# Performance work log

Hardware: AMD Instinct MI355X
Metric: run time of the kernel (lower is better)

Reference implementation:

```python
import jax, jax.numpy as jnp
import numpy as np

B, LQ, DM, DFFN, NL, NH, NP = 4, 13294, 256, 1024, 4, 8, 4
HD = DM // NH
SHAPES = np.array([[100, 100], [50, 50], [25, 25], [13, 13]], dtype=np.int64)


def _ln(x, g, b):
    m = x.mean(-1, keepdims=True)
    v = ((x - m) ** 2).mean(-1, keepdims=True)
    return (x - m) / jnp.sqrt(v + 1e-5) * g + b


def _ms_deform(value, loc, aw, shapes):
    # value: [B, Lv, NH, HD]; loc: [B, Lq, NH, NL, NP, 2]; aw: [B, Lq, NH, NL, NP]
    Bn, Lq = loc.shape[0], loc.shape[1]
    offs = np.concatenate([[0], np.cumsum(shapes[:, 0] * shapes[:, 1])])
    out = jnp.zeros((Bn, NH, Lq, HD), value.dtype)
    for l in range(NL):
        H, W = int(shapes[l, 0]), int(shapes[l, 1])
        val = value[:, offs[l]:offs[l + 1]].transpose(0, 2, 1, 3)  # [B,NH,HW,HD]
        # grid_sample align_corners=False convention: pixel = norm*size - 0.5
        x = (loc[:, :, :, l, :, 0] * W - 0.5).transpose(0, 2, 1, 3).reshape(Bn, NH, Lq * NP)
        y = (loc[:, :, :, l, :, 1] * H - 0.5).transpose(0, 2, 1, 3).reshape(Bn, NH, Lq * NP)
        x0 = jnp.floor(x); y0 = jnp.floor(y)
        fx = x - x0; fy = y - y0
        acc = jnp.zeros((Bn, NH, Lq * NP, HD), value.dtype)
        for dy, dx in ((0, 0), (0, 1), (1, 0), (1, 1)):
            xi = x0 + dx; yi = y0 + dy
            w = (fx if dx else 1.0 - fx) * (fy if dy else 1.0 - fy)
            valid = (xi >= 0) & (xi < W) & (yi >= 0) & (yi < H)  # zero padding
            idx = (jnp.clip(yi, 0, H - 1) * W + jnp.clip(xi, 0, W - 1)).astype(jnp.int32)
            g = jnp.take_along_axis(val, idx[..., None], axis=2)  # [B,NH,Lq*NP,HD]
            acc = acc + g * (w * valid)[..., None]
        a = aw[:, :, :, l].transpose(0, 2, 1, 3).reshape(Bn, NH, Lq * NP)
        out = out + (acc * a[..., None]).reshape(Bn, NH, Lq, NP, HD).sum(3)
    return out.transpose(0, 2, 1, 3).reshape(Bn, Lq, NH * HD)


def _forward(src, pos, reference_points, shapes, Wv, bv, Ws, bs, Wa, ba, Wo, bo,
             W1, b1, W2, b2, g1, be1, g2, be2):
    Bn, Lq, _ = src.shape
    q = src + pos
    value = (src @ Wv + bv).reshape(Bn, Lq, NH, HD)
    off = (q @ Ws + bs).reshape(Bn, Lq, NH, NL, NP, 2)
    aw = jax.nn.softmax((q @ Wa + ba).reshape(Bn, Lq, NH, NL * NP), axis=-1)
    aw = aw.reshape(Bn, Lq, NH, NL, NP)
    norm = jnp.asarray(np.ascontiguousarray(shapes[:, ::-1]), jnp.float32)  # (W,H) per level
    loc = reference_points[:, :, None, :, None, :] + off / norm[None, None, None, :, None, :]
    attn = _ms_deform(value, loc, aw, shapes) @ Wo + bo
    x = _ln(src + attn, g1, be1)
    h = jax.nn.relu(x @ W1 + b1)
    return _ln(x + h @ W2 + b2, g2, be2)


def setup_inputs():
    key = jax.random.key(0)
    ks = jax.random.split(key, 12)

    def lin(k, i, o):
        k1, k2 = jax.random.split(k)
        return (0.02 * jax.random.normal(k1, (i, o), jnp.float32),
                0.02 * jax.random.normal(k2, (o,), jnp.float32))

    Wv, bv = lin(ks[0], DM, DM)
    Ws, bs = lin(ks[1], DM, NH * NL * NP * 2)
    Wa, ba = lin(ks[2], DM, NH * NL * NP)
    Wo, bo = lin(ks[3], DM, DM)
    W1, b1 = lin(ks[4], DM, DFFN)
    W2, b2 = lin(ks[5], DFFN, DM)
    lsi = np.concatenate([[0], np.cumsum(SHAPES[:, 0] * SHAPES[:, 1])[:-1]])
    return {
        "src": jax.random.normal(ks[6], (B, LQ, DM), jnp.float32),
        "pos": jax.random.normal(ks[7], (B, LQ, DM), jnp.float32),
        "reference_points": jax.random.uniform(ks[8], (B, LQ, NL, 2), jnp.float32),
        "spatial_shapes": jnp.asarray(SHAPES),
        "level_start_index": jnp.asarray(lsi),
        "Wv": Wv, "bv": bv, "Ws": Ws, "bs": bs, "Wa": Wa, "ba": ba,
        "Wo": Wo, "bo": bo, "W1": W1, "b1": b1, "W2": W2, "b2": b2,
        "g1": jnp.ones((DM,), jnp.float32), "be1": jnp.zeros((DM,), jnp.float32),
        "g2": jnp.ones((DM,), jnp.float32), "be2": jnp.zeros((DM,), jnp.float32),
    }


def reference(src, pos, reference_points, spatial_shapes, level_start_index,
              Wv, bv, Ws, bs, Wa, ba, Wo, bo, W1, b1, W2, b2, g1, be1, g2, be2):
    shapes = np.asarray(spatial_shapes)
    return _forward(src, pos, reference_points, shapes, Wv, bv, Ws, bs, Wa, ba,
                    Wo, bo, W1, b1, W2, b2, g1, be1, g2, be2)
```

## Files before the change

kernel.cpp:

```cpp
#include <hip/hip_runtime.h>


#define LQn   13294
#define MREAL 53176
#define MP    53248
#define MHALF 26588

typedef __attribute__((ext_vector_type(8))) short short8;
typedef __attribute__((ext_vector_type(4))) short short4v;
typedef __attribute__((ext_vector_type(4))) float f32x4;
typedef __attribute__((ext_vector_type(2))) float f32x2;

__device__ __forceinline__ short f2bf(float f) {
    unsigned u = __float_as_uint(f);
    unsigned r = (u + 0x7FFFu + ((u >> 16) & 1u)) >> 16;
    return (short)r;
}
__device__ __forceinline__ float bf2f(short b) {
    return __uint_as_float(((unsigned)(unsigned short)b) << 16);
}
__device__ __forceinline__ f32x2 bf2x2(unsigned r) {
    f32x2 o;
    o.x = __uint_as_float(r << 16);
    o.y = __uint_as_float(r & 0xffff0000u);
    return o;
}

#define GLOAD16(gp, lp)                                                        \
    __builtin_amdgcn_global_load_lds(                                          \
        (const __attribute__((address_space(1))) void*)(gp),                   \
        (__attribute__((address_space(3))) void*)(lp), 16, 0, 0)

__global__ __launch_bounds__(256) void prep_all(
    const float* __restrict__ Wv, const float* __restrict__ Ws,
    const float* __restrict__ Wa, const float* __restrict__ Wo,
    const float* __restrict__ W1, const float* __restrict__ W2,
    const float* __restrict__ bs, const float* __restrict__ ba,
    const float* __restrict__ src, const float* __restrict__ pos,
    short* __restrict__ WvT, short* __restrict__ WsaT,
    short* __restrict__ WoT, short* __restrict__ W1T,
    short* __restrict__ W2T, float* __restrict__ bsa,
    short* __restrict__ q_bf, short* __restrict__ src_bf) {
    const int bid = blockIdx.x, tid = threadIdx.x;
    if (bid >= 2945) {
        const int i = (bid - 2945) * 256 + tid;
        if (i < MREAL * 32) {
            const float4 a0 = ((const float4*)src)[i * 2];
            const float4 a1 = ((const float4*)src)[i * 2 + 1];
            const float4 b0 = ((const float4*)pos)[i * 2];
            const float4 b1 = ((const float4*)pos)[i * 2 + 1];
            short8 o, o2;
            o[0] = f2bf(a0.x + b0.x); o[1] = f2bf(a0.y + b0.y);
            o[2] = f2bf(a0.z + b0.z); o[3] = f2bf(a0.w + b0.w);
            o[4] = f2bf(a1.x + b1.x); o[5] = f2bf(a1.y + b1.y);
            o[6] = f2bf(a1.z + b1.z); o[7] = f2bf(a1.w + b1.w);
            o2[0] = f2bf(a0.x); o2[1] = f2bf(a0.y);
            o2[2] = f2bf(a0.z); o2[3] = f2bf(a0.w);
            o2[4] = f2bf(a1.x); o2[5] = f2bf(a1.y);
            o2[6] = f2bf(a1.z); o2[7] = f2bf(a1.w);
            ((short8*)q_bf)[i] = o;
            ((short8*)src_bf)[i] = o2;
        }
        return;
    }
    const float* W; short* WT; int K, N, base;
    if (bid < 256)       { W = Wv; WT = WvT;              K = 256;  N = 256;  base = 0; }
    else if (bid < 512)  { W = Ws; WT = WsaT;             K = 256;  N = 256;  base = 256; }
    else if (bid < 640)  { W = Wa; WT = WsaT + 256 * 256; K = 256;  N = 128;  base = 512; }
    else if (bid < 896)  { W = Wo; WT = WoT;              K = 256;  N = 256;  base = 640; }
    else if (bid < 1920) { W = W1; WT = W1T;              K = 256;  N = 1024; base = 896; }
    else if (bid < 2944) { W = W2; WT = W2T;              K = 1024; N = 256;  base = 1920; }
    else {
        if (tid < 256) bsa[tid] = bs[tid];
        else if (tid < 384) bsa[tid] = ba[tid - 256];
        return;
    }
    const int i = (bid - base) * 256 + tid;
    const int n = i / K, k = i - n * K;
    WT[i] = f2bf(W[(size_t)k * N + n]);
}

template <int EPI, int NT>
__device__ __forceinline__ void gemm_body(short* lA, short* lB,
                                          const short* __restrict__ Ab,
                                          const short* __restrict__ BT,
                                          const float* __restrict__ bias,
                                          void* C, int d,
                                          int M, int K, int N,
                                          int ldb, int ldc) {
    const int c = d & 7, j = d >> 3;
    const int jg = j / NT;
    const int m0 = (c + 8 * jg) * 128;
    const int n0 = (j - jg * NT) * 128;
    const int t = threadIdx.x;
    const int wid = t >> 6, lane = t & 63;
    const int wr = wid >> 1, wc = wid & 1;
    const int quad = lane >> 4, l16 = lane & 15;

    f32x4 acc[4][4];
#pragma unroll
    for (int i = 0; i < 4; ++i)
#pragma unroll
        for (int jj = 0; jj < 4; ++jj) acc[i][jj] = (f32x4){0.f, 0.f, 0.f, 0.f};

    const int grow = wid * 32 + (lane >> 2);
    const int gcol = (lane & 3) * 8;
    auto stage = [&](int buf, int k0) {
        GLOAD16(Ab + (size_t)(m0 + grow) * K + k0 + gcol,
                &lA[buf * 4096 + (wid * 32) * 32]);
        GLOAD16(Ab + (size_t)(m0 + grow + 16) * K + k0 + gcol,
                &lA[buf * 4096 + (wid * 32 + 16) * 32]);
        GLOAD16(BT + (size_t)(n0 + grow) * ldb + k0 + gcol,
                &lB[buf * 4096 + (wid * 32) * 32]);
        GLOAD16(BT + (size_t)(n0 + grow + 16) * ldb + k0 + gcol,
                &lB[buf * 4096 + (wid * 32 + 16) * 32]);
    };
    stage(0, 0);
    __syncthreads();
    int cur = 0;
    for (int k0 = 0; k0 < K; k0 += 32) {
        if (k0 + 32 < K) stage(cur ^ 1, k0 + 32);
        short8 af[4], bfr[4];
#pragma unroll
        for (int mi = 0; mi < 4; ++mi)
            af[mi] = *(const short8*)&lA[cur * 4096 + (wr * 64 + mi * 16 + l16) * 32 + quad * 8];
#pragma unroll
        for (int ni = 0; ni < 4; ++ni)
            bfr[ni] = *(const short8*)&lB[cur * 4096 + (wc * 64 + ni * 16 + l16) * 32 + quad * 8];
#pragma unroll
        for (int mi = 0; mi < 4; ++mi)
#pragma unroll
            for (int ni = 0; ni < 4; ++ni)
                acc[mi][ni] = __builtin_amdgcn_mfma_f32_16x16x32_bf16(
                    af[mi], bfr[ni], acc[mi][ni], 0, 0, 0);
        __syncthreads();
        cur ^= 1;
    }

    short* lflat = lA;
#pragma unroll
    for (int p = 0; p < 2; ++p) {
        if (wc == p) {
#pragma unroll
            for (int ni = 0; ni < 4; ++ni) {
                const int lc = ni * 16 + l16;
                const float bia = bias[n0 + p * 64 + lc];
#pragma unroll
                for (int mi = 0; mi < 4; ++mi)
#pragma unroll
                    for (int r = 0; r < 4; ++r) {
                        const int lr = wr * 64 + mi * 16 + quad * 4 + r;
                        float v = acc[mi][ni][r] + bia;
                        if (EPI == 2) v = fmaxf(v, 0.f);
                        lflat[lr * 64 + (lc ^ ((lr & 7) << 3))] = f2bf(v);
                    }
            }
        }
        __syncthreads();
#pragma unroll
        for (int i = 0; i < 4; ++i) {
            const int chunk = i * 256 + t;
            const int row = chunk >> 3;
            const int c8 = (chunk & 7) * 8;
            const int gr = m0 + row;
            if (gr < M) {
                const short8 v8 =
                    *(const short8*)&lflat[row * 64 + (c8 ^ ((row & 7) << 3))];
                const int gcl = n0 + p * 64 + c8;
                if (EPI == 5) {
                    const int b = gr / LQn, s = gr - b * LQn;
                    const int hh = gcl >> 5, dd = gcl & 31;
                    *(short8*)&((short*)C)[(((size_t)b * 8 + hh) * LQn + s) * 32 + dd] = v8;
                } else {
                    *(short8*)&((short*)C)[(size_t)gr * ldc + gcl] = v8;
                }
            }
        }
        __syncthreads();
    }
}

template <int EPI, int NT>
__global__ __launch_bounds__(256) void gemm_bt(const short* __restrict__ Ab,
                                               const short* __restrict__ BT,
                                               const float* __restrict__ bias,
                                               void* C, int M, int K, int N,
                                               int ldb, int ldc) {
    __shared__ short sA[2 * 128 * 32];
    __shared__ short sB[2 * 128 * 32];
    gemm_body<EPI, NT>(sA, sB, Ab, BT, bias, C, blockIdx.x, M, K, N, ldb, ldc);
}

__global__ __launch_bounds__(256) void gemm12(const short* __restrict__ src_bf,
                                              const short* __restrict__ WvT,
                                              const float* __restrict__ bv,
                                              short* __restrict__ value_h,
                                              const short* __restrict__ q_bf,
                                              const short* __restrict__ WsaT,
                                              const float* __restrict__ bsa,
                                              short* __restrict__ offaw) {
    __shared__ short sA[2 * 128 * 32];
    __shared__ short sB[2 * 128 * 32];
    if (blockIdx.x < 832)
        gemm_body<5, 2>(sA, sB, src_bf, WvT, bv, value_h, blockIdx.x,
                        MREAL, 256, 256, 256, 256);
    else
        gemm_body<1, 3>(sA, sB, q_bf, WsaT, bsa, offaw, blockIdx.x - 832,
                        MREAL, 256, 384, 256, 384);
}

template <int EPI>
__global__ __launch_bounds__(512) void gemm_ln(const short* __restrict__ Ab,
                                               const short* __restrict__ BT,
                                               const float* __restrict__ bias,
                                               const void* __restrict__ resid,
                                               void* __restrict__ out,
                                               const float* __restrict__ g,
                                               const float* __restrict__ be,
                                               int M, int K, int resbf) {
    const int t = threadIdx.x;
    const int m0 = blockIdx.x * 64;
    const int wid = t >> 6, lane = t & 63;
    const int wr = wid >> 2, wc = wid & 3;
    const int quad = lane >> 4, l16 = lane & 15;

    __shared__ short lA[2][64 * 32];
    __shared__ short lB[2][256 * 32];
    __shared__ float2 part[64][4];
    __shared__ float2 stats[64];

    f32x4 acc[2][4];
#pragma unroll
    for (int i = 0; i < 2; ++i)
#pragma unroll
        for (int j = 0; j < 4; ++j) acc[i][j] = (f32x4){0.f, 0.f, 0.f, 0.f};

    const int gb_row = wid * 32 + (lane >> 2);
    const int gcol8 = (lane & 3) * 8;
    auto stage = [&](int buf, int k0) {
        if (wid < 4)
            GLOAD16(Ab + (size_t)(m0 + wid * 16 + (lane >> 2)) * K + k0 + gcol8,
                    &lA[buf][(wid * 16) * 32]);
        GLOAD16(BT + (size_t)gb_row * K + k0 + gcol8,
                &lB[buf][(wid * 32) * 32]);
        GLOAD16(BT + (size_t)(gb_row + 16) * K + k0 + gcol8,
                &lB[buf][(wid * 32 + 16) * 32]);
    };
    stage(0, 0);
    __syncthreads();
    int cur = 0;
    for (int k0 = 0; k0 < K; k0 += 32) {
        if (k0 + 32 < K) stage(cur ^ 1, k0 + 32);
        short8 af[2], bfr[4];
#pragma unroll
        for (int mi = 0; mi < 2; ++mi)
            af[mi] = *(const short8*)&lA[cur][(wr * 32 + mi * 16 + l16) * 32 + quad * 8];
#pragma unroll
        for (int ni = 0; ni < 4; ++ni)
            bfr[ni] = *(const short8*)&lB[cur][(wc * 64 + ni * 16 + l16) * 32 + quad * 8];
#pragma unroll
        for (int mi = 0; mi < 2; ++mi)
#pragma unroll
            for (int ni = 0; ni < 4; ++ni)
                acc[mi][ni] = __builtin_amdgcn_mfma_f32_16x16x32_bf16(
                    af[mi], bfr[ni], acc[mi][ni], 0, 0, 0);
        __syncthreads();
        cur ^= 1;
    }

    float biasv[4], gv[4], bev[4];
    int gcs[4];
#pragma unroll
    for (int ni = 0; ni < 4; ++ni) {
        gcs[ni] = wc * 64 + ni * 16 + l16;
        biasv[ni] = bias[gcs[ni]];
        gv[ni] = g[gcs[ni]];
        bev[ni] = be[gcs[ni]];
    }
#pragma unroll
    for (int mi = 0; mi < 2; ++mi) {
#pragma unroll
        for (int r = 0; r < 4; ++r) {
            const int lr = wr * 32 + mi * 16 + quad * 4 + r;
            const int gr = m0 + lr;
            const bool ok = (gr < M);
            float s1 = 0.f, s2 = 0.f;
#pragma unroll
            for (int ni = 0; ni < 4; ++ni) {
                float v = acc[mi][ni][r] + biasv[ni];
                if (ok) {
                    if (resbf)
                        v += bf2f(((const short*)resid)[(size_t)gr * 256 + gcs[ni]]);
                    else
                        v += ((const float*)resid)[(size_t)gr * 256 + gcs[ni]];
                }
                acc[mi][ni][r] = v;
                s1 += v;
                s2 += v * v;
            }
#pragma unroll
            for (int o = 1; o < 16; o <<= 1) {
                s1 += __shfl_xor(s1, o);
                s2 += __shfl_xor(s2, o);
            }
            if (l16 == 0) part[lr][wc] = make_float2(s1, s2);
        }
    }
    __syncthreads();
    if (t < 64) {
        float s1 = 0.f, s2 = 0.f;
#pragma unroll
        for (int w = 0; w < 4; ++w) {
            const float2 p = part[t][w];
            s1 += p.x;
            s2 += p.y;
        }
        const float mean = s1 * (1.0f / 256.0f);
        const float var = s2 * (1.0f / 256.0f) - mean * mean;
        stats[t] = make_float2(mean, rsqrtf(var + 1e-5f));
    }
    __syncthreads();

    if (EPI == 0) {
        short* lflat = (short*)lA;
#pragma unroll
        for (int p = 0; p < 4; ++p) {
            if (wc == p) {
#pragma unroll
                for (int mi = 0; mi < 2; ++mi)
#pragma unroll
                    for (int r = 0; r < 4; ++r) {
                        const int lr = wr * 32 + mi * 16 + quad * 4 + r;
                        const float2 st = stats[lr];
#pragma unroll
                        for (int ni = 0; ni < 4; ++ni) {
                            const int lc = ni * 16 + l16;
                            const float v =
                                (acc[mi][ni][r] - st.x) * st.y * gv[ni] + bev[ni];
                            lflat[lr * 64 + (lc ^ ((lr & 7) << 3))] = f2bf(v);
                        }
                    }
            }
            __syncthreads();
            {
                const int row = t >> 3;
                const int c8 = (t & 7) * 8;
                const int gr = m0 + row;
                if (gr < M) {
                    const short8 v8 =
                        *(const short8*)&lflat[row * 64 + (c8 ^ ((row & 7) << 3))];
                    *(short8*)&((short*)out)[(size_t)gr * 256 + p * 64 + c8] = v8;
                }
            }
            __syncthreads();
        }
    } else {
#pragma unroll
        for (int mi = 0; mi < 2; ++mi) {
#pragma unroll
            for (int r = 0; r < 4; ++r) {
                const int lr = wr * 32 + mi * 16 + quad * 4 + r;
                const int gr = m0 + lr;
                if (gr < M) {
                    const float2 st = stats[lr];
#pragma unroll
                    for (int ni = 0; ni < 4; ++ni) {
                        const float v =
                            (acc[mi][ni][r] - st.x) * st.y * gv[ni] + bev[ni];
                        ((float*)out)[(size_t)gr * 256 + gcs[ni]] = v;
                    }
                }
            }
        }
    }
}

__global__ __launch_bounds__(256) void sample_k(const short* __restrict__ value,
                                                const short* __restrict__ offaw,
                                                const float* __restrict__ refp,
                                                short* __restrict__ attn,
                                                int nwg) {
    int wg = blockIdx.x;
    {
        const int q = nwg >> 3, r = nwg & 7;
        const int xcd = wg & 7, idx = wg >> 3;
        wg = (xcd < r ? xcd * (q + 1) : r * (q + 1) + (xcd - r) * q) + idx;
    }
    const int tid = threadIdx.x;
    const int grp = wg * 16 + (tid >> 4);
    const int s16 = tid & 15;
    const int l = s16 >> 2, sub = s16 & 3;
    const int row = grp >> 3, h = grp & 7;
    const int b = row / LQn;
    const int L = (l == 0) ? 100 : (l == 1) ? 50 : (l == 2) ? 25 : 13;
    const int O = (l == 0) ? 0 : (l == 1) ? 10000 : (l == 2) ? 12500 : 13125;
    const float Lf = (float)L;

    const short* op = offaw + (size_t)row * 384 + h * 32;
    const short* ap = offaw + (size_t)row * 384 + 256 + h * 16;

    const short4v alog = *(const short4v*)(ap + l * 4);
    float lg[4];
#pragma unroll
    for (int j = 0; j < 4; ++j) lg[j] = bf2f(alog[j]);
    float m = fmaxf(fmaxf(lg[0], lg[1]), fmaxf(lg[2], lg[3]));
    m = fmaxf(m, __shfl_xor(m, 4));
    m = fmaxf(m, __shfl_xor(m, 8));
    float s = 0.f;
#pragma unroll
    for (int j = 0; j < 4; ++j) { lg[j] = __expf(lg[j] - m); s += lg[j]; }
    s += __shfl_xor(s, 4);
    s += __shfl_xor(s, 8);
    const float inv = 1.f / s;

    const float2 rxy = *(const float2*)(refp + (size_t)row * 8 + l * 2);
    const short8 ov = *(const short8*)(op + l * 8);
    const short* vlev = value + ((size_t)(b * 8 + h) * LQn + O) * 32 + sub * 8;

    f32x2 acc2[4];
#pragma unroll
    for (int j = 0; j < 4; ++j) acc2[j] = (f32x2){0.f, 0.f};

#pragma unroll 2
    for (int p = 0; p < 4; ++p) {
        const float x = fmaf(rxy.x, Lf, bf2f(ov[p * 2 + 0]) - 0.5f);
        const float y = fmaf(rxy.y, Lf, bf2f(ov[p * 2 + 1]) - 0.5f);
        const float xf = floorf(x), yf = floorf(y);
        const int ix = (int)xf, iy = (int)yf;
        const float fx = x - xf, fy = y - yf;
        const float aw = lg[p] * inv;
        const float vx0 = ((unsigned)ix < (unsigned)L) ? 1.f : 0.f;
        const float vx1 = ((unsigned)(ix + 1) < (unsigned)L) ? 1.f : 0.f;
        const float vy0 = ((unsigned)iy < (unsigned)L) ? 1.f : 0.f;
        const float vy1 = ((unsigned)(iy + 1) < (unsigned)L) ? 1.f : 0.f;
        const float gx0 = (1.f - fx) * aw, gx1 = fx * aw;
        const float w00 = gx0 * (1.f - fy) * vx0 * vy0;
        const float w10 = gx1 * (1.f - fy) * vx1 * vy0;
        const float w01 = gx0 * fy * vx0 * vy1;
        const float w11 = gx1 * fy * vx1 * vy1;
        const int ix0 = min(max(ix, 0), L - 1);
        const int ix1 = min(max(ix + 1, 0), L - 1);
        const int iy0 = min(max(iy, 0), L - 1);
        const int iy1 = min(max(iy + 1, 0), L - 1);
        const int ro0 = iy0 * L, ro1 = iy1 * L;
        const uint4 c00 = *(const uint4*)(vlev + ((ro0 + ix0) << 5));
        const uint4 c10 = *(const uint4*)(vlev + ((ro0 + ix1) << 5));
        const uint4 c01 = *(const uint4*)(vlev + ((ro1 + ix0) << 5));
        const uint4 c11 = *(const uint4*)(vlev + ((ro1 + ix1) << 5));
        const unsigned* p00 = (const unsigned*)&c00;
        const unsigned* p10 = (const unsigned*)&c10;
        const unsigned* p01 = (const unsigned*)&c01;
        const unsigned* p11 = (const unsigned*)&c11;
#pragma unroll
        for (int j = 0; j < 4; ++j)
            acc2[j] += w00 * bf2x2(p00[j]) + w10 * bf2x2(p10[j]) +
                       w01 * bf2x2(p01[j]) + w11 * bf2x2(p11[j]);
    }

    float acc[8];
#pragma unroll
    for (int j = 0; j < 4; ++j) {
        acc[j * 2] = acc2[j].x;
        acc[j * 2 + 1] = acc2[j].y;
    }
#pragma unroll
    for (int j = 0; j < 8; ++j) {
        acc[j] += __shfl_xor(acc[j], 4);
        acc[j] += __shfl_xor(acc[j], 8);
    }

    if (l == 0) {
        short8 o;
#pragma unroll
        for (int j = 0; j < 8; ++j) o[j] = f2bf(acc[j]);
        *(short8*)(attn + (size_t)row * 256 + h * 32 + sub * 8) = o;
    }
}

extern "C" void kernel_launch(void* const* d_in, const int* in_sizes, int n_in,
                              void* d_out, int out_size, void* d_ws, size_t ws_size,
                              hipStream_t stream) {
    (void)in_sizes; (void)n_in; (void)out_size;
    const float* src  = (const float*)d_in[0];
    const float* pos  = (const float*)d_in[1];
    const float* refp = (const float*)d_in[2];
    const float* Wv = (const float*)d_in[5];
    const float* bv = (const float*)d_in[6];
    const float* Ws = (const float*)d_in[7];
    const float* bs = (const float*)d_in[8];
    const float* Wa = (const float*)d_in[9];
    const float* ba = (const float*)d_in[10];
    const float* Wo = (const float*)d_in[11];
    const float* bo = (const float*)d_in[12];
    const float* W1 = (const float*)d_in[13];
    const float* b1 = (const float*)d_in[14];
    const float* W2 = (const float*)d_in[15];
    const float* b2 = (const float*)d_in[16];
    const float* g1 = (const float*)d_in[17];
    const float* be1 = (const float*)d_in[18];
    const float* g2 = (const float*)d_in[19];
    const float* be2 = (const float*)d_in[20];

    char* ws = (char*)d_ws;
    size_t off = 0;
    auto take = [&](size_t bytes) {
        char* p = ws + off;
        off += (bytes + 255) & ~(size_t)255;
        return p;
    };
    short* WvT  = (short*)take(256 * 256 * 2);
    short* WsaT = (short*)take(384 * 256 * 2);
    short* WoT  = (short*)take(256 * 256 * 2);
    short* W1T  = (short*)take(1024 * 256 * 2);
    short* W2T  = (short*)take(256 * 1024 * 2);
    float* bsa  = (float*)take(384 * 4);

    const size_t SZ_VH = (size_t)MP * 256 * 2;
    const size_t SZ_OF = (size_t)MP * 384 * 2;
    const size_t SZ_H  = (size_t)MP * 1024 * 2;
    const size_t SZ_HX = SZ_H - (SZ_OF + 2 * SZ_VH);

    short* value_h = (short*)take(SZ_VH);
    short* offaw   = (short*)take(SZ_OF);
    short* attn_bf = (short*)take(SZ_VH);

    const size_t rem = (off <= ws_size) ? ws_size - off : 0;
    const bool cfgFull = rem >= SZ_VH + SZ_HX + 512;
    const bool cfgA    = !cfgFull && rem >= SZ_VH + 256;
    short* src_bf;
    int resbf_g4;
    if (cfgFull) {
        src_bf = (short*)take(SZ_VH);
        (void)take(SZ_HX);
        resbf_g4 = 1;
    } else if (cfgA) {
        src_bf = (short*)take(SZ_VH);
        resbf_g4 = 1;
    } else {
        src_bf = offaw;
        resbf_g4 = 0;
    }

    short* q_bf = attn_bf;
    short* x_bf = value_h;
    short* h    = offaw;
    float* z    = (float*)d_out;

    prep_all<<<9593, 256, 0, stream>>>(Wv, Ws, Wa, Wo, W1, W2, bs, ba, src, pos,
                                       WvT, WsaT, WoT, W1T, W2T, bsa, q_bf,
                                       src_bf);
    gemm12<<<2080, 256, 0, stream>>>(src_bf, WvT, bv, value_h,
                                     q_bf, WsaT, bsa, offaw);
    {
        const int nwg = (MREAL * 8) / 16;
        sample_k<<<nwg, 256, 0, stream>>>(value_h, offaw, refp, attn_bf, nwg);
    }
    gemm_ln<0><<<MP / 64, 512, 0, stream>>>(attn_bf, WoT, bo,
                                            resbf_g4 ? (const void*)src_bf
                                                     : (const void*)src,
                                            x_bf, g1, be1, MREAL, 256, resbf_g4);
    if (cfgFull) {
        gemm_bt<2, 8><<<3328, 256, 0, stream>>>(
            x_bf, W1T, b1, h, MREAL, 256, 1024, 256, 1024);
        gemm_ln<1><<<MP / 64, 512, 0, stream>>>(h, W2T, b2, x_bf, z, g2, be2,
                                                MREAL, 1024, 1);
    } else {
        for (int half = 0; half < 2; ++half) {
            const size_t ro = (size_t)half * MHALF;
            gemm_bt<2, 8><<<1664, 256, 0, stream>>>(
                x_bf + ro * 256, W1T, b1, h, MHALF, 256, 1024, 256, 1024);
            gemm_ln<1><<<(MHALF + 63) / 64, 512, 0, stream>>>(
                h, W2T, b2, x_bf + ro * 256, z + ro * 256, g2, be2, MHALF, 1024,
                1);
        }
    }
}
```

Baseline: 366.4 us.

## Fuse FFN up-projection, ReLU, down-projection and LayerNorm into one kernel

Replaces the separate W1 GEMM (writing a 1024-wide bf16 hidden buffer to global memory) and the W2 GEMM+LayerNorm kernel with a single kernel. Each 64-row block computes hidden chunks of 128 columns into shared memory and immediately accumulates them into the W2 output, avoiding the large hidden-tensor round trip and the workspace-size branches. In exchange, x rows are read directly from global per MFMA step, weights are restreamed for every row block, and the per-block tile is small (64 rows), which may lower MFMA efficiency relative to the standalone tiled GEMM.

```diff
diff --git a/kernel.cpp b/kernel.cpp
--- a/kernel.cpp
+++ b/kernel.cpp
@@ -4,7 +4,6 @@
 #define LQn   13294
 #define MREAL 53176
 #define MP    53248
-#define MHALF 26588
 
 typedef __attribute__((ext_vector_type(8))) short short8;
 typedef __attribute__((ext_vector_type(4))) short short4v;
@@ -151,7 +150,6 @@
                     for (int r = 0; r < 4; ++r) {
                         const int lr = wr * 64 + mi * 16 + quad * 4 + r;
                         float v = acc[mi][ni][r] + bia;
-                        if (EPI == 2) v = fmaxf(v, 0.f);
                         lflat[lr * 64 + (lc ^ ((lr & 7) << 3))] = f2bf(v);
                     }
             }
@@ -180,17 +178,6 @@
     }
 }
 
-template <int EPI, int NT>
-__global__ __launch_bounds__(256) void gemm_bt(const short* __restrict__ Ab,
-                                               const short* __restrict__ BT,
-                                               const float* __restrict__ bias,
-                                               void* C, int M, int K, int N,
-                                               int ldb, int ldc) {
-    __shared__ short sA[2 * 128 * 32];
-    __shared__ short sB[2 * 128 * 32];
-    gemm_body<EPI, NT>(sA, sB, Ab, BT, bias, C, blockIdx.x, M, K, N, ldb, ldc);
-}
-
 __global__ __launch_bounds__(256) void gemm12(const short* __restrict__ src_bf,
                                               const short* __restrict__ WvT,
                                               const float* __restrict__ bv,
@@ -209,15 +196,14 @@
                         MREAL, 256, 384, 256, 384);
 }
 
-template <int EPI>
-__global__ __launch_bounds__(512) void gemm_ln(const short* __restrict__ Ab,
-                                               const short* __restrict__ BT,
-                                               const float* __restrict__ bias,
-                                               const void* __restrict__ resid,
-                                               void* __restrict__ out,
-                                               const float* __restrict__ g,
-                                               const float* __restrict__ be,
-                                               int M, int K, int resbf) {
+__global__ __launch_bounds__(512) void gemm_ln0(const short* __restrict__ Ab,
+                                                const short* __restrict__ BT,
+                                                const float* __restrict__ bias,
+                                                const void* __restrict__ resid,
+                                                void* __restrict__ out,
+                                                const float* __restrict__ g,
+                                                const float* __restrict__ be,
+                                                int M, int K, int resbf) {
     const int t = threadIdx.x;
     const int m0 = blockIdx.x * 64;
     const int wid = t >> 6, lane = t & 63;
@@ -321,54 +307,216 @@
     }
     __syncthreads();
 
-    if (EPI == 0) {
-        short* lflat = (short*)lA;
-#pragma unroll
-        for (int p = 0; p < 4; ++p) {
-            if (wc == p) {
-#pragma unroll
-                for (int mi = 0; mi < 2; ++mi)
-#pragma unroll
-                    for (int r = 0; r < 4; ++r) {
-                        const int lr = wr * 32 + mi * 16 + quad * 4 + r;
-                        const float2 st = stats[lr];
-#pragma unroll
-                        for (int ni = 0; ni < 4; ++ni) {
-                            const int lc = ni * 16 + l16;
-                            const float v =
-                                (acc[mi][ni][r] - st.x) * st.y * gv[ni] + bev[ni];
-                            lflat[lr * 64 + (lc ^ ((lr & 7) << 3))] = f2bf(v);
-                        }
-                    }
-            }
-            __syncthreads();
-            {
-                const int row = t >> 3;
-                const int c8 = (t & 7) * 8;
-                const int gr = m0 + row;
-                if (gr < M) {
-                    const short8 v8 =
-                        *(const short8*)&lflat[row * 64 + (c8 ^ ((row & 7) << 3))];
-                    *(short8*)&((short*)out)[(size_t)gr * 256 + p * 64 + c8] = v8;
-                }
-            }
-            __syncthreads();
-        }
-    } else {
-#pragma unroll
-        for (int mi = 0; mi < 2; ++mi) {
-#pragma unroll
-            for (int r = 0; r < 4; ++r) {
-                const int lr = wr * 32 + mi * 16 + quad * 4 + r;
-                const int gr = m0 + lr;
-                if (gr < M) {
+    short* lflat = (short*)lA;
+#pragma unroll
+    for (int p = 0; p < 4; ++p) {
+        if (wc == p) {
+#pragma unroll
+            for (int mi = 0; mi < 2; ++mi)
+#pragma unroll
+                for (int r = 0; r < 4; ++r) {
+                    const int lr = wr * 32 + mi * 16 + quad * 4 + r;
                     const float2 st = stats[lr];
 #pragma unroll
                     for (int ni = 0; ni < 4; ++ni) {
+                        const int lc = ni * 16 + l16;
                         const float v =
                             (acc[mi][ni][r] - st.x) * st.y * gv[ni] + bev[ni];
-                        ((float*)out)[(size_t)gr * 256 + gcs[ni]] = v;
+                        lflat[lr * 64 + (lc ^ ((lr & 7) << 3))] = f2bf(v);
                     }
+                }
+        }
+        __syncthreads();
+        {
+            const int row = t >> 3;
+            const int c8 = (t & 7) * 8;
+            const int gr = m0 + row;
+            if (gr < M) {
+                const short8 v8 =
+                    *(const short8*)&lflat[row * 64 + (c8 ^ ((row & 7) << 3))];
+                *(short8*)&((short*)out)[(size_t)gr * 256 + p * 64 + c8] = v8;
+            }
+        }
+        __syncthreads();
+    }
+}
+
+__global__ __launch_bounds__(512) void ffn_fused(const short* __restrict__ x,
+                                                 const short* __restrict__ W1T,
+                                                 const float* __restrict__ b1,
+                                                 const short* __restrict__ W2T,
+                                                 const float* __restrict__ b2,
+                                                 float* __restrict__ z,
+                                                 const float* __restrict__ g,
+                                                 const float* __restrict__ be,
+                                                 int M) {
+    const int t = threadIdx.x;
+    const int m0 = blockIdx.x * 64;
+    const int wid = t >> 6, lane = t & 63;
+    const int wr = wid >> 2, wc = wid & 3;
+    const int quad = lane >> 4, l16 = lane & 15;
+    const int s_row = lane >> 2, s_col8 = (lane & 3) * 8;
+
+    __shared__ short lW1[2][128 * 32];
+    __shared__ short lW2[2][256 * 32];
+    __shared__ short lH[64 * 128];
+    __shared__ float2 part[64][4];
+    __shared__ float2 stats[64];
+
+    f32x4 acc2[2][4];
+#pragma unroll
+    for (int i = 0; i < 2; ++i)
+#pragma unroll
+        for (int j = 0; j < 4; ++j) acc2[i][j] = (f32x4){0.f, 0.f, 0.f, 0.f};
+
+    int xrow[2];
+#pragma unroll
+    for (int mi = 0; mi < 2; ++mi)
+        xrow[mi] = min(m0 + wr * 32 + mi * 16 + l16, M - 1);
+
+    for (int nc = 0; nc < 8; ++nc) {
+        f32x4 acc1[2][2];
+#pragma unroll
+        for (int i = 0; i < 2; ++i)
+#pragma unroll
+            for (int j = 0; j < 2; ++j) acc1[i][j] = (f32x4){0.f, 0.f, 0.f, 0.f};
+
+        auto stage1 = [&](int buf, int kk) {
+            GLOAD16(W1T + (size_t)(nc * 128 + wid * 16 + s_row) * 256 + kk * 32 + s_col8,
+                    &lW1[buf][(wid * 16) * 32]);
+        };
+        stage1(0, 0);
+        __syncthreads();
+        int cur = 0;
+#pragma unroll
+        for (int kk = 0; kk < 8; ++kk) {
+            if (kk < 7) stage1(cur ^ 1, kk + 1);
+            short8 ax[2];
+#pragma unroll
+            for (int mi = 0; mi < 2; ++mi)
+                ax[mi] = *(const short8*)&x[(size_t)xrow[mi] * 256 + kk * 32 + quad * 8];
+            short8 bw[2];
+#pragma unroll
+            for (int ni = 0; ni < 2; ++ni)
+                bw[ni] = *(const short8*)&lW1[cur][((wc & 3) * 32 + ni * 16 + l16) * 32 + quad * 8];
+#pragma unroll
+            for (int mi = 0; mi < 2; ++mi)
+#pragma unroll
+                for (int ni = 0; ni < 2; ++ni)
+                    acc1[mi][ni] = __builtin_amdgcn_mfma_f32_16x16x32_bf16(
+                        ax[mi], bw[ni], acc1[mi][ni], 0, 0, 0);
+            __syncthreads();
+            cur ^= 1;
+        }
+#pragma unroll
+        for (int mi = 0; mi < 2; ++mi)
+#pragma unroll
+            for (int ni = 0; ni < 2; ++ni) {
+                const int col = wc * 32 + ni * 16 + l16;
+                const float bia = b1[nc * 128 + col];
+#pragma unroll
+                for (int r = 0; r < 4; ++r) {
+                    const int row = wr * 32 + mi * 16 + quad * 4 + r;
+                    const float v = fmaxf(acc1[mi][ni][r] + bia, 0.f);
+                    lH[row * 128 + ((((col >> 3) ^ (row & 7)) << 3) | (col & 7))] =
+                        f2bf(v);
+                }
+            }
+        __syncthreads();
+        auto stage2 = [&](int buf, int kk) {
+            GLOAD16(W2T + (size_t)(wid * 32 + s_row) * 1024 + nc * 128 + kk * 32 + s_col8,
+                    &lW2[buf][(wid * 32) * 32]);
+            GLOAD16(W2T + (size_t)(wid * 32 + 16 + s_row) * 1024 + nc * 128 + kk * 32 + s_col8,
+                    &lW2[buf][(wid * 32 + 16) * 32]);
+        };
+        stage2(0, 0);
+        __syncthreads();
+        cur = 0;
+#pragma unroll
+        for (int kk = 0; kk < 4; ++kk) {
+            if (kk < 3) stage2(cur ^ 1, kk + 1);
+            short8 ah[2];
+#pragma unroll
+            for (int mi = 0; mi < 2; ++mi) {
+                const int row = wr * 32 + mi * 16 + l16;
+                ah[mi] = *(const short8*)&lH[row * 128 +
+                                             (((kk * 4 + quad) ^ (row & 7)) << 3)];
+            }
+            short8 bw2[4];
+#pragma unroll
+            for (int ni = 0; ni < 4; ++ni)
+                bw2[ni] = *(const short8*)&lW2[cur][(wc * 64 + ni * 16 + l16) * 32 + quad * 8];
+#pragma unroll
+            for (int mi = 0; mi < 2; ++mi)
+#pragma unroll
+                for (int ni = 0; ni < 4; ++ni)
+                    acc2[mi][ni] = __builtin_amdgcn_mfma_f32_16x16x32_bf16(
+                        ah[mi], bw2[ni], acc2[mi][ni], 0, 0, 0);
+            __syncthreads();
+            cur ^= 1;
+        }
+    }
+
+    float biasv[4], gv[4], bev[4];
+    int gcs[4];
+#pragma unroll
+    for (int ni = 0; ni < 4; ++ni) {
+        gcs[ni] = wc * 64 + ni * 16 + l16;
+        biasv[ni] = b2[gcs[ni]];
+        gv[ni] = g[gcs[ni]];
+        bev[ni] = be[gcs[ni]];
+    }
+#pragma unroll
+    for (int mi = 0; mi < 2; ++mi) {
+#pragma unroll
+        for (int r = 0; r < 4; ++r) {
+            const int lr = wr * 32 + mi * 16 + quad * 4 + r;
+            const int gr = m0 + lr;
+            const bool ok = (gr < M);
+            float s1 = 0.f, s2 = 0.f;
+#pragma unroll
+            for (int ni = 0; ni < 4; ++ni) {
+                float v = acc2[mi][ni][r] + biasv[ni];
+                if (ok) v += bf2f(x[(size_t)gr * 256 + gcs[ni]]);
+                acc2[mi][ni][r] = v;
+                s1 += v;
+                s2 += v * v;
+            }
+#pragma unroll
+            for (int o = 1; o < 16; o <<= 1) {
+                s1 += __shfl_xor(s1, o);
+                s2 += __shfl_xor(s2, o);
+            }
+            if (l16 == 0) part[lr][wc] = make_float2(s1, s2);
+        }
+    }
+    __syncthreads();
+    if (t < 64) {
+        float s1 = 0.f, s2 = 0.f;
+#pragma unroll
+        for (int w = 0; w < 4; ++w) {
+            const float2 p = part[t][w];
+            s1 += p.x;
+            s2 += p.y;
+        }
+        const float mean = s1 * (1.0f / 256.0f);
+        const float var = s2 * (1.0f / 256.0f) - mean * mean;
+        stats[t] = make_float2(mean, rsqrtf(var + 1e-5f));
+    }
+    __syncthreads();
+#pragma unroll
+    for (int mi = 0; mi < 2; ++mi) {
+#pragma unroll
+        for (int r = 0; r < 4; ++r) {
+            const int lr = wr * 32 + mi * 16 + quad * 4 + r;
+            const int gr = m0 + lr;
+            if (gr < M) {
+                const float2 st = stats[lr];
+#pragma unroll
+                for (int ni = 0; ni < 4; ++ni) {
+                    const float v =
+                        (acc2[mi][ni][r] - st.x) * st.y * gv[ni] + bev[ni];
+                    z[(size_t)gr * 256 + gcs[ni]] = v;
                 }
             }
         }
@@ -517,23 +665,15 @@
 
     const size_t SZ_VH = (size_t)MP * 256 * 2;
     const size_t SZ_OF = (size_t)MP * 384 * 2;
-    const size_t SZ_H  = (size_t)MP * 1024 * 2;
-    const size_t SZ_HX = SZ_H - (SZ_OF + 2 * SZ_VH);
 
     short* value_h = (short*)take(SZ_VH);
     short* offaw   = (short*)take(SZ_OF);
     short* attn_bf = (short*)take(SZ_VH);
 
     const size_t rem = (off <= ws_size) ? ws_size - off : 0;
-    const bool cfgFull = rem >= SZ_VH + SZ_HX + 512;
-    const bool cfgA    = !cfgFull && rem >= SZ_VH + 256;
     short* src_bf;
     int resbf_g4;
-    if (cfgFull) {
-        src_bf = (short*)take(SZ_VH);
-        (void)take(SZ_HX);
-        resbf_g4 = 1;
-    } else if (cfgA) {
+    if (rem >= SZ_VH + 256) {
         src_bf = (short*)take(SZ_VH);
         resbf_g4 = 1;
     } else {
@@ -543,7 +683,6 @@
 
     short* q_bf = attn_bf;
     short* x_bf = value_h;
-    short* h    = offaw;
     float* z    = (float*)d_out;
 
     prep_all<<<9593, 256, 0, stream>>>(Wv, Ws, Wa, Wo, W1, W2, bs, ba, src, pos,
@@ -555,23 +694,10 @@
         const int nwg = (MREAL * 8) / 16;
         sample_k<<<nwg, 256, 0, stream>>>(value_h, offaw, refp, attn_bf, nwg);
     }
-    gemm_ln<0><<<MP / 64, 512, 0, stream>>>(attn_bf, WoT, bo,
-                                            resbf_g4 ? (const void*)src_bf
-                                                     : (const void*)src,
-                                            x_bf, g1, be1, MREAL, 256, resbf_g4);
-    if (cfgFull) {
-        gemm_bt<2, 8><<<3328, 256, 0, stream>>>(
-            x_bf, W1T, b1, h, MREAL, 256, 1024, 256, 1024);
-        gemm_ln<1><<<MP / 64, 512, 0, stream>>>(h, W2T, b2, x_bf, z, g2, be2,
-                                                MREAL, 1024, 1);
-    } else {
-        for (int half = 0; half < 2; ++half) {
-            const size_t ro = (size_t)half * MHALF;
-            gemm_bt<2, 8><<<1664, 256, 0, stream>>>(
-                x_bf + ro * 256, W1T, b1, h, MHALF, 256, 1024, 256, 1024);
-            gemm_ln<1><<<(MHALF + 63) / 64, 512, 0, stream>>>(
-                h, W2T, b2, x_bf + ro * 256, z + ro * 256, g2, be2, MHALF, 1024,
-                1);
-        }
-    }
-}
+    gemm_ln0<<<MP / 64, 512, 0, stream>>>(attn_bf, WoT, bo,
+                                          resbf_g4 ? (const void*)src_bf
+                                                   : (const void*)src,
+                                          x_bf, g1, be1, MREAL, 256, resbf_g4);
+    ffn_fused<<<MP / 64, 512, 0, stream>>>(x_bf, W1T, b1, W2T, b2, z, g2, be2,
+                                           MREAL);
+}
```

Measured after the change: 406.4 us. 1.11x slower.
